# Kernel optimization log

Hardware: AMD Instinct MI355X
Metric: run time of the kernel (lower is better)

## Reference

```python
import jax, jax.numpy as jnp
import numpy as np

B, T, P, U = 2, 50, 5111, 64


def setup_inputs() -> dict:
    key = jax.random.key(0)
    ks = jax.random.split(key, 12)
    data_target = jax.random.randint(ks[0], (B, T), 0, P)
    data_cor = jax.random.randint(ks[1], (B, T), 0, 2)
    # X: bi-LSTM max-pooled problem encodings [P, 2U]
    X = jax.random.normal(ks[2], (P, 2 * U), dtype=jnp.float32) * 0.1
    # cos_X: cosine similarity of X with itself (as in call_encode)
    norm = jnp.sqrt(jnp.sum(X * X, axis=1))
    cos_X = (X @ X.T) / (norm[:, None] * norm[None, :])
    # causal lower-triangular aggregation mask [T, T]
    trimatrix = jnp.tril(jnp.ones((T, T), dtype=jnp.float32))
    # frozen embedding2 table [2, 4U]
    emb2 = jax.random.uniform(ks[3], (2, 4 * U), minval=-1.0, maxval=1.0, dtype=jnp.float32)
    # LSTM params (keras gate order i,f,c,o), input dim 4U
    s = 0.1549193338
    Wk = jax.random.uniform(ks[4], (4 * U, 4 * U), minval=-s, maxval=s, dtype=jnp.float32)
    Wr = jax.random.normal(ks[5], (U, 4 * U), dtype=jnp.float32) * 0.05  # orthogonal-ish stand-in
    bl = jnp.concatenate([jnp.zeros((U,)), jnp.ones((U,)), jnp.zeros((2 * U,))]).astype(jnp.float32)  # unit forget bias
    s1 = 0.1732050808
    W1 = jax.random.uniform(ks[6], (3 * U, 50), minval=-s1, maxval=s1, dtype=jnp.float32)
    b1 = jnp.zeros((50,), dtype=jnp.float32)
    s2 = 0.3429971703
    W2 = jax.random.uniform(ks[7], (50, 1), minval=-s2, maxval=s2, dtype=jnp.float32)
    b2 = jnp.zeros((1,), dtype=jnp.float32)
    return {"data_target": data_target, "data_cor": data_cor, "num_pro": P,
            "X": X, "cos_X": cos_X, "trimatrix": trimatrix, "emb2": emb2,
            "Wk": Wk, "Wr": Wr, "bl": bl, "W1": W1, "b1": b1, "W2": W2, "b2": b2}


def _lstm(x, Wk, Wr, bl):
    # x: [B, T, D] -> h: [B, T, U]; keras LSTM math, gate order i,f,g,o
    u = Wr.shape[0]
    xT = jnp.swapaxes(x, 0, 1)  # [T, B, D]
    h0 = jnp.zeros((x.shape[0], u), x.dtype)
    c0 = jnp.zeros((x.shape[0], u), x.dtype)

    def step(carry, xt):
        h, c = carry
        z = xt @ Wk + h @ Wr + bl
        i, f, g, o = jnp.split(z, 4, axis=-1)
        c = jax.nn.sigmoid(f) * c + jax.nn.sigmoid(i) * jnp.tanh(g)
        h = jax.nn.sigmoid(o) * jnp.tanh(c)
        return (h, c), h

    _, hs = jax.lax.scan(step, (h0, c0), xT)
    return jnp.swapaxes(hs, 0, 1)


def reference(data_target, data_cor, num_pro, X, cos_X, trimatrix, emb2, Wk, Wr, bl, W1, b1, W2, b2):
    # one_hot @ X == gather
    t_X = X[data_target]                             # [B,T,2U]
    t_X = jnp.concatenate([t_X, t_X], axis=-1)       # [B,T,4U]
    xt = t_X * emb2[data_cor]                        # [B,T,4U]
    ht = _lstm(xt, Wk, Wr, bl)                       # [B,T,U]
    # attention aggregation: a[b,t,p] = cos_X[target[b,t], p]
    a = cos_X[data_target]                           # [B,T,P]
    # ajhj[b,s,p,u] = sum_t trimatrix[t,s] * a[b,t,p] * ht[b,t,u]
    ajhj = jnp.einsum('btp,btu,ts->bspu', a, ht, trimatrix)  # [B,T,P,U]
    XX = jnp.broadcast_to(X[None, None], (ajhj.shape[0], ajhj.shape[1], num_pro, X.shape[1]))
    hatt = jnp.concatenate([ajhj, XX], axis=-1)      # [B,T,P,3U]
    r = jax.nn.relu(hatt @ W1 + b1)                  # [B,T,P,50]
    r = r @ W2 + b2                                  # [B,T,P,1]
    return r
```

## Files before the change

### kernel.cpp

```cpp
#include <hip/hip_runtime.h>
#include <math.h>

#define B_ 2
#define T_ 50
#define P_ 5111
#define U_ 64
#define SC_ 10
#define CH_ 5
#define NQ_ 1278
#define XWTB_ 254
#define OUT_BASE_ 256
#define OUTB_ 200
#define GRID_ (OUT_BASE_ + OUTB_)
#define MAGIC_ 0x5EED1E55

typedef float v2f __attribute__((ext_vector_type(2)));

#define QPERM(x, ctrl)                                                        \
  __int_as_float(__builtin_amdgcn_mov_dpp(__float_as_int(x), (ctrl), 0xf, 0xf, true))

__device__ __forceinline__ float ld_coh(const float* p) {
  return __hip_atomic_load(p, __ATOMIC_RELAXED, __HIP_MEMORY_SCOPE_AGENT);
}
__device__ __forceinline__ void st_coh(float* p, float v) {
  __hip_atomic_store(p, v, __ATOMIC_RELAXED, __HIP_MEMORY_SCOPE_AGENT);
}
__device__ __forceinline__ void wait_flag(const int* f) {
  while (__hip_atomic_load(f, __ATOMIC_RELAXED, __HIP_MEMORY_SCOPE_AGENT) != MAGIC_)
    __builtin_amdgcn_s_sleep(2);
}
__device__ __forceinline__ void set_flag(int* f) {
  __hip_atomic_store(f, MAGIC_, __ATOMIC_RELAXED, __HIP_MEMORY_SCOPE_AGENT);
}

union SMem {
  struct {
    float H[T_ + 1][64];
    union {
      float ZXs[T_][256];
      float W1s[64 * 50];
    } z;
  } lstm;
  float xe[256];
  float xrow[4][128];
  struct { float G[T_ * 50]; float W2s[50]; int tgt[T_]; } outr;
};

__device__ __forceinline__ void lstm_role(
    int b, SMem& sm, const float* ZX, const float* Wr, const float* bl,
    const float* W1, float* G, const int* zxflag, int* gflag) {
  const int k   = threadIdx.x;
  const int g   = k & 3;
  const int u   = k >> 2;
  const int col = g * 64 + u;

  v2f w2[32];
#pragma unroll
  for (int i = 0; i < 32; ++i) {
    v2f t; t.x = Wr[(2 * i) * 256 + col]; t.y = Wr[(2 * i + 1) * 256 + col];
    w2[i] = t;
  }
  const float blv = bl[col];
  if (k < 64) sm.lstm.H[0][k] = 0.f;
  if (k < T_) wait_flag(&zxflag[b * T_ + k]);
  __syncthreads();

  {
    float r[T_];
#pragma unroll
    for (int t = 0; t < T_; ++t) r[t] = ld_coh(&ZX[(b * T_ + t) * 256 + k]);
#pragma unroll
    for (int t = 0; t < T_; ++t) sm.lstm.z.ZXs[t][k] = r[t];
  }
  float w1r[13];
#pragma unroll
  for (int j = 0; j < 13; ++j) {
    const int i = k + j * 256;
    w1r[j] = (i < 64 * 50) ? W1[i] : 0.f;
  }
  __syncthreads();

  float c = 0.f;
  __builtin_amdgcn_s_setprio(1);
  for (int t = 0; t < T_; ++t) {
    const float zcur = sm.lstm.z.ZXs[t][col];
    const float4* h4 = (const float4*)&sm.lstm.H[t][0];
    v2f a0 = {0.f, 0.f}, a1 = {0.f, 0.f}, a2 = {0.f, 0.f}, a3 = {0.f, 0.f};
#pragma unroll
    for (int q = 0; q < 16; ++q) {
      const float4 hq = h4[q];
      v2f hlo; hlo.x = hq.x; hlo.y = hq.y;
      v2f hhi; hhi.x = hq.z; hhi.y = hq.w;
      if (q & 1) {
        a2 = __builtin_elementwise_fma(hlo, w2[2 * q], a2);
        a3 = __builtin_elementwise_fma(hhi, w2[2 * q + 1], a3);
      } else {
        a0 = __builtin_elementwise_fma(hlo, w2[2 * q], a0);
        a1 = __builtin_elementwise_fma(hhi, w2[2 * q + 1], a1);
      }
    }
    const v2f as = (a0 + a2) + (a1 + a3);
    const float z = as.x + as.y + zcur + blv;
    const bool isg2 = (g == 2);
    const float arg = isg2 ? (2.f * z) : (-z);
    const float e   = __expf(arg);
    const float v   = __fdividef(1.f, 1.f + e);
    const float res = isg2 ? fmaf(-2.f, v, 1.f) : v;
    const float v1 = QPERM(res, 177);
    const float v2 = QPERM(res, 78);
    const float v3 = QPERM(res, 27);
    const float ig = (g == 0) ? res : (g == 1) ? v1 : (g == 2) ? v2 : v3;
    const float fg = (g == 1) ? res : (g == 0) ? v1 : (g == 3) ? v2 : v3;
    const float gg = (g == 2) ? res : (g == 3) ? v1 : (g == 0) ? v2 : v3;
    const float og = (g == 3) ? res : (g == 2) ? v1 : (g == 1) ? v2 : v3;
    c = fmaf(fg, c, ig * gg);
    const float th = fmaf(-2.f, __fdividef(1.f, 1.f + __expf(2.f * c)), 1.f);
    if (g == 0) sm.lstm.H[t + 1][u] = og * th;
    __syncthreads();
  }
  __builtin_amdgcn_s_setprio(0);

#pragma unroll
  for (int j = 0; j < 13; ++j) {
    const int i = k + j * 256;
    if (i < 64 * 50) sm.lstm.z.W1s[i] = w1r[j];
  }
  __syncthreads();

  const v2f* W1_2 = (const v2f*)sm.lstm.z.W1s;
  for (int task = k; task < T_ * 25; task += 256) {
    const int t  = task / 25;
    const int jp = task % 25;
    const float* hrow = &sm.lstm.H[t + 1][0];
    v2f acc = {0.f, 0.f};
#pragma unroll
    for (int u2 = 0; u2 < 64; ++u2) {
      v2f hb; hb.x = hrow[u2]; hb.y = hrow[u2];
      acc = __builtin_elementwise_fma(hb, W1_2[u2 * 25 + jp], acc);
    }
    st_coh(&G[b * (T_ * 50) + 2 * task],     acc.x);
    st_coh(&G[b * (T_ * 50) + 2 * task + 1], acc.y);
  }
  __syncthreads();
  if (k == 0) set_flag(&gflag[b]);
}

__device__ __forceinline__ void prod_role(
    int blk, SMem& sm, const int* tgt, const int* cor, const float* X,
    const float* emb2, const float* Wk, const float* W1, const float* b1,
    float* ZX, float* XWT, int* zxflag, int* quadflag) {
  const int k = threadIdx.x;

  if (blk - 2 < B_ * T_) {
    const int bt = blk - 2;
    const int t_ = tgt[bt], c_ = cor[bt];
    sm.xe[k] = X[t_ * 128 + (k & 127)] * emb2[c_ * 256 + k];
    __syncthreads();
    float z = 0.f;
#pragma unroll 8
    for (int d = 0; d < 256; ++d)
      z = fmaf(sm.xe[d], Wk[d * 256 + k], z);
    st_coh(&ZX[bt * 256 + k], z);
    __syncthreads();
    if (k == 0) set_flag(&zxflag[bt]);
  }

  const int sub = k >> 6, lane = k & 63;
  const int stripe = (blk - 102 + XWTB_) % XWTB_;
  for (int q = stripe; q < NQ_; q += XWTB_) {
    const int p = q * 4 + sub;
    if (p < P_) {
      sm.xrow[sub][lane]      = X[p * 128 + lane];
      sm.xrow[sub][64 + lane] = X[p * 128 + 64 + lane];
    }
    __syncthreads();
    if (p < P_ && lane < 50) {
      float acc = b1[lane];
#pragma unroll 16
      for (int u = 0; u < 128; ++u)
        acc = fmaf(sm.xrow[sub][u], W1[(64 + u) * 50 + lane], acc);
      st_coh(&XWT[lane * P_ + p], acc);
    }
    __syncthreads();
    if (k == 0) set_flag(&quadflag[q]);
  }
}

template <int CH>
__device__ __forceinline__ void out_body(
    int pc, int b, SMem& sm, const int* tgt, const float* cosX,
    const float* G, const float* XWT, const float* W2, const float* b2,
    float* out, const int* gflag, const int* quadflag) {
  constexpr int s_lo = CH * SC_;
  constexpr int s_hi = s_lo + SC_;
  const int tid = threadIdx.x;
  const int p   = pc * 256 + tid;
  const bool act = (p < P_);

  if (tid < 50) {
    sm.outr.W2s[tid] = W2[tid];
    sm.outr.tgt[tid] = tgt[b * T_ + tid];
  }
  __syncthreads();

  float av[T_ - s_lo];
#pragma unroll
  for (int t = s_lo; t < T_; ++t)
    av[t - s_lo] = act ? cosX[sm.outr.tgt[t] * P_ + p] : 0.f;

  if (tid < 64) {
    const int q = pc * 64 + tid;
    if (q < NQ_) wait_flag(&quadflag[q]);
  }
  __syncthreads();

  v2f S2[25];
#pragma unroll
  for (int jj = 0; jj < 25; ++jj) {
    v2f t2;
    t2.x = act ? ld_coh(&XWT[(2 * jj) * P_ + p]) : 0.f;
    t2.y = act ? ld_coh(&XWT[(2 * jj + 1) * P_ + p]) : 0.f;
    S2[jj] = t2;
  }

  if (tid == 0) wait_flag(&gflag[b]);
  __syncthreads();
  for (int i = s_lo * 50 + tid; i < T_ * 50; i += 256)
    sm.outr.G[i] = ld_coh(&G[b * T_ * 50 + i]);
  __syncthreads();

#pragma unroll
  for (int t = T_ - 1; t >= s_hi; --t) {
    const v2f* G2 = (const v2f*)&sm.outr.G[t * 50];
    v2f av2; av2.x = av[t - s_lo]; av2.y = av[t - s_lo];
#pragma unroll
    for (int jj = 0; jj < 25; ++jj)
      S2[jj] = __builtin_elementwise_fma(av2, G2[jj], S2[jj]);
  }

  const v2f* W2_2 = (const v2f*)sm.outr.W2s;
  const float b2v = b2[0];
  const v2f zero2 = {0.f, 0.f};
#pragma unroll
  for (int s = s_hi - 1; s >= s_lo; --s) {
    const v2f* G2 = (const v2f*)&sm.outr.G[s * 50];
    v2f av2; av2.x = av[s - s_lo]; av2.y = av[s - s_lo];
    v2f acc2; acc2.x = b2v; acc2.y = 0.f;
#pragma unroll
    for (int jj = 0; jj < 25; ++jj) {
      S2[jj] = __builtin_elementwise_fma(av2, G2[jj], S2[jj]);
      const v2f r = __builtin_elementwise_max(S2[jj], zero2);
      acc2 = __builtin_elementwise_fma(r, W2_2[jj], acc2);
    }
    if (act) out[(b * T_ + s) * P_ + p] = acc2.x + acc2.y;
  }
}

__global__ __launch_bounds__(256) void mega_kernel(
    const int* __restrict__ tgt, const int* __restrict__ cor,
    const float* __restrict__ X, const float* __restrict__ cosX,
    const float* __restrict__ emb2, const float* __restrict__ Wk,
    const float* __restrict__ Wr, const float* __restrict__ bl,
    const float* __restrict__ W1, const float* __restrict__ b1,
    const float* __restrict__ W2, const float* __restrict__ b2,
    float* __restrict__ ZX, float* __restrict__ G, float* __restrict__ XWT,
    int* __restrict__ zxflag, int* __restrict__ gflag,
    int* __restrict__ quadflag, float* __restrict__ out) {
  __shared__ __align__(16) SMem sm;
  const int blk = blockIdx.x;

  if (blk < B_) {
    lstm_role(blk, sm, ZX, Wr, bl, W1, G, zxflag, gflag);
    return;
  }
  if (blk < OUT_BASE_) {
    prod_role(blk, sm, tgt, cor, X, emb2, Wk, W1, b1, ZX, XWT, zxflag, quadflag);
    return;
  }
  const int obi = blk - OUT_BASE_;
  const int pc  = obi % 20;
  const int b   = (obi / 20) & 1;
  switch (obi / 40) {
    case 0: out_body<0>(pc, b, sm, tgt, cosX, G, XWT, W2, b2, out, gflag, quadflag); break;
    case 1: out_body<1>(pc, b, sm, tgt, cosX, G, XWT, W2, b2, out, gflag, quadflag); break;
    case 2: out_body<2>(pc, b, sm, tgt, cosX, G, XWT, W2, b2, out, gflag, quadflag); break;
    case 3: out_body<3>(pc, b, sm, tgt, cosX, G, XWT, W2, b2, out, gflag, quadflag); break;
    default: out_body<4>(pc, b, sm, tgt, cosX, G, XWT, W2, b2, out, gflag, quadflag); break;
  }
}

extern "C" void kernel_launch(void* const* d_in, const int* in_sizes, int n_in,
                              void* d_out, int out_size, void* d_ws, size_t ws_size,
                              hipStream_t stream) {
  const int*   tgt  = (const int*)d_in[0];
  const int*   cor  = (const int*)d_in[1];
  const float* X    = (const float*)d_in[3];
  const float* cosX = (const float*)d_in[4];
  const float* emb2 = (const float*)d_in[6];
  const float* Wk   = (const float*)d_in[7];
  const float* Wr   = (const float*)d_in[8];
  const float* bl   = (const float*)d_in[9];
  const float* W1   = (const float*)d_in[10];
  const float* b1   = (const float*)d_in[11];
  const float* W2   = (const float*)d_in[12];
  const float* b2   = (const float*)d_in[13];
  float* out = (float*)d_out;

  float* ws  = (float*)d_ws;
  float* ZX  = ws;
  float* G   = ws + 25600;
  float* XWT = ws + 30600;
  int*   fl  = (int*)(ws + 286150);
  int* zxflag   = fl;
  int* gflag    = fl + 100;
  int* quadflag = fl + 102;

  mega_kernel<<<dim3(GRID_), dim3(256), 0, stream>>>(
      tgt, cor, X, cosX, emb2, Wk, Wr, bl, W1, b1, W2, b2,
      ZX, G, XWT, zxflag, gflag, quadflag, out);
}
```

Baseline: 217.0 us.

## Compute LSTM recurrence on two waves with two gate columns per thread

Restructures the serial LSTM recurrence so 128 threads (two waves) each compute two gate columns instead of 256 threads computing one. The gate exchange shrinks to a single DPP permute per pair. The other two waves load W1 into registers, stay in step with the per-timestep barriers, then stage W1 to shared memory. This is meant to cut the latency of each recurrent step, which sits on the critical path, though each thread now does twice the FMAs and holds twice the weight registers. A launch-bounds hint of two blocks per SM is also added, which can limit register allocation.

```diff
diff --git a/kernel.cpp b/kernel.cpp
--- a/kernel.cpp
+++ b/kernel.cpp
@@ -49,18 +49,8 @@
 __device__ __forceinline__ void lstm_role(
     int b, SMem& sm, const float* ZX, const float* Wr, const float* bl,
     const float* W1, float* G, const int* zxflag, int* gflag) {
-  const int k   = threadIdx.x;
-  const int g   = k & 3;
-  const int u   = k >> 2;
-  const int col = g * 64 + u;
-
-  v2f w2[32];
-#pragma unroll
-  for (int i = 0; i < 32; ++i) {
-    v2f t; t.x = Wr[(2 * i) * 256 + col]; t.y = Wr[(2 * i + 1) * 256 + col];
-    w2[i] = t;
-  }
-  const float blv = bl[col];
+  const int k = threadIdx.x;
+
   if (k < 64) sm.lstm.H[0][k] = 0.f;
   if (k < T_) wait_flag(&zxflag[b * T_ + k]);
   __syncthreads();
@@ -72,60 +62,86 @@
 #pragma unroll
     for (int t = 0; t < T_; ++t) sm.lstm.z.ZXs[t][k] = r[t];
   }
-  float w1r[13];
-#pragma unroll
-  for (int j = 0; j < 13; ++j) {
-    const int i = k + j * 256;
-    w1r[j] = (i < 64 * 50) ? W1[i] : 0.f;
-  }
-  __syncthreads();
-
-  float c = 0.f;
-  __builtin_amdgcn_s_setprio(1);
-  for (int t = 0; t < T_; ++t) {
-    const float zcur = sm.lstm.z.ZXs[t][col];
-    const float4* h4 = (const float4*)&sm.lstm.H[t][0];
-    v2f a0 = {0.f, 0.f}, a1 = {0.f, 0.f}, a2 = {0.f, 0.f}, a3 = {0.f, 0.f};
-#pragma unroll
-    for (int q = 0; q < 16; ++q) {
-      const float4 hq = h4[q];
-      v2f hlo; hlo.x = hq.x; hlo.y = hq.y;
-      v2f hhi; hhi.x = hq.z; hhi.y = hq.w;
-      if (q & 1) {
-        a2 = __builtin_elementwise_fma(hlo, w2[2 * q], a2);
-        a3 = __builtin_elementwise_fma(hhi, w2[2 * q + 1], a3);
-      } else {
-        a0 = __builtin_elementwise_fma(hlo, w2[2 * q], a0);
-        a1 = __builtin_elementwise_fma(hhi, w2[2 * q + 1], a1);
+
+  if (k < 128) {
+    const int u    = k >> 1;
+    const int pair = k & 1;
+    const int colA = pair * 128 + u;
+    const int colB = pair * 128 + 64 + u;
+
+    v2f wA[32], wB[32];
+#pragma unroll
+    for (int i = 0; i < 32; ++i) {
+      v2f ta; ta.x = Wr[(2 * i) * 256 + colA]; ta.y = Wr[(2 * i + 1) * 256 + colA];
+      wA[i] = ta;
+      v2f tb; tb.x = Wr[(2 * i) * 256 + colB]; tb.y = Wr[(2 * i + 1) * 256 + colB];
+      wB[i] = tb;
+    }
+    const float blvA = bl[colA];
+    const float blvB = bl[colB];
+    __syncthreads();
+
+    float c = 0.f;
+    __builtin_amdgcn_s_setprio(1);
+    for (int t = 0; t < T_; ++t) {
+      const float zAcur = sm.lstm.z.ZXs[t][colA];
+      const float zBcur = sm.lstm.z.ZXs[t][colB];
+      const float4* h4 = (const float4*)&sm.lstm.H[t][0];
+      v2f a0 = {0.f, 0.f}, a1 = {0.f, 0.f}, a2 = {0.f, 0.f}, a3 = {0.f, 0.f};
+      v2f b0 = {0.f, 0.f}, b1 = {0.f, 0.f}, b2 = {0.f, 0.f}, b3 = {0.f, 0.f};
+#pragma unroll
+      for (int q = 0; q < 16; ++q) {
+        const float4 hq = h4[q];
+        v2f hlo; hlo.x = hq.x; hlo.y = hq.y;
+        v2f hhi; hhi.x = hq.z; hhi.y = hq.w;
+        if (q & 1) {
+          a2 = __builtin_elementwise_fma(hlo, wA[2 * q], a2);
+          a3 = __builtin_elementwise_fma(hhi, wA[2 * q + 1], a3);
+          b2 = __builtin_elementwise_fma(hlo, wB[2 * q], b2);
+          b3 = __builtin_elementwise_fma(hhi, wB[2 * q + 1], b3);
+        } else {
+          a0 = __builtin_elementwise_fma(hlo, wA[2 * q], a0);
+          a1 = __builtin_elementwise_fma(hhi, wA[2 * q + 1], a1);
+          b0 = __builtin_elementwise_fma(hlo, wB[2 * q], b0);
+          b1 = __builtin_elementwise_fma(hhi, wB[2 * q + 1], b1);
+        }
       }
-    }
-    const v2f as = (a0 + a2) + (a1 + a3);
-    const float z = as.x + as.y + zcur + blv;
-    const bool isg2 = (g == 2);
-    const float arg = isg2 ? (2.f * z) : (-z);
-    const float e   = __expf(arg);
-    const float v   = __fdividef(1.f, 1.f + e);
-    const float res = isg2 ? fmaf(-2.f, v, 1.f) : v;
-    const float v1 = QPERM(res, 177);
-    const float v2 = QPERM(res, 78);
-    const float v3 = QPERM(res, 27);
-    const float ig = (g == 0) ? res : (g == 1) ? v1 : (g == 2) ? v2 : v3;
-    const float fg = (g == 1) ? res : (g == 0) ? v1 : (g == 3) ? v2 : v3;
-    const float gg = (g == 2) ? res : (g == 3) ? v1 : (g == 0) ? v2 : v3;
-    const float og = (g == 3) ? res : (g == 2) ? v1 : (g == 1) ? v2 : v3;
-    c = fmaf(fg, c, ig * gg);
-    const float th = fmaf(-2.f, __fdividef(1.f, 1.f + __expf(2.f * c)), 1.f);
-    if (g == 0) sm.lstm.H[t + 1][u] = og * th;
-    __syncthreads();
-  }
-  __builtin_amdgcn_s_setprio(0);
-
-#pragma unroll
-  for (int j = 0; j < 13; ++j) {
-    const int i = k + j * 256;
-    if (i < 64 * 50) sm.lstm.z.W1s[i] = w1r[j];
-  }
-  __syncthreads();
+      const v2f asA = (a0 + a2) + (a1 + a3);
+      const v2f asB = (b0 + b2) + (b1 + b3);
+      const float zA = asA.x + asA.y + zAcur + blvA;
+      const float zB = asB.x + asB.y + zBcur + blvB;
+
+      const bool isg2 = (pair == 1);
+      const float argA = isg2 ? (2.f * zA) : (-zA);
+      const float eA   = __expf(argA);
+      const float vA   = __fdividef(1.f, 1.f + eA);
+      const float resA = isg2 ? fmaf(-2.f, vA, 1.f) : vA;
+      const float eB   = __expf(-zB);
+      const float resB = __fdividef(1.f, 1.f + eB);
+
+      const float xA = QPERM(resA, 177);
+      const float xB = QPERM(resB, 177);
+      const float ig = isg2 ? xA : resA;
+      const float fg = isg2 ? xB : resB;
+      const float gg = isg2 ? resA : xA;
+
+      c = fmaf(fg, c, ig * gg);
+      const float th = fmaf(-2.f, __fdividef(1.f, 1.f + __expf(2.f * c)), 1.f);
+      if (isg2) sm.lstm.H[t + 1][u] = resB * th;
+      __syncthreads();
+    }
+    __builtin_amdgcn_s_setprio(0);
+    __syncthreads();
+  } else {
+    float w1r[25];
+#pragma unroll
+    for (int j = 0; j < 25; ++j) w1r[j] = W1[(k - 128) + j * 128];
+    __syncthreads();
+    for (int t = 0; t < T_; ++t) __syncthreads();
+#pragma unroll
+    for (int j = 0; j < 25; ++j) sm.lstm.z.W1s[(k - 128) + j * 128] = w1r[j];
+    __syncthreads();
+  }
 
   const v2f* W1_2 = (const v2f*)sm.lstm.z.W1s;
   for (int task = k; task < T_ * 25; task += 256) {
@@ -256,7 +272,7 @@
   }
 }
 
-__global__ __launch_bounds__(256) void mega_kernel(
+__global__ __launch_bounds__(256, 2) void mega_kernel(
     const int* __restrict__ tgt, const int* __restrict__ cor,
     const float* __restrict__ X, const float* __restrict__ cosX,
     const float* __restrict__ emb2, const float* __restrict__ Wk,
```

New measurement: 225.2 us. +3.8%, slower.

## Split producer work into a separate kernel launch instead of flag-synchronized roles

Applied to the files above, without the earlier changes.

Moves the ZX projection and X·W1 precompute out of the persistent mega-kernel into a standalone producer kernel with one block per row or quad. The consumer kernel then runs the LSTM and output blocks without waiting on zxflag or quadflag, relying on stream ordering instead. This removes spin-waits and coherent atomic loads and stores, and gives the XWT precompute many more blocks. The cost is an extra kernel launch and losing overlap between producer and consumer work. The gflag handshake between LSTM and output blocks remains.

```diff
diff --git a/kernel.cpp b/kernel.cpp
--- a/kernel.cpp
+++ b/kernel.cpp
@@ -8,10 +8,6 @@
 #define SC_ 10
 #define CH_ 5
 #define NQ_ 1278
-#define XWTB_ 254
-#define OUT_BASE_ 256
-#define OUTB_ 200
-#define GRID_ (OUT_BASE_ + OUTB_)
 #define MAGIC_ 0x5EED1E55
 
 typedef float v2f __attribute__((ext_vector_type(2)));
@@ -33,7 +29,47 @@
   __hip_atomic_store(f, MAGIC_, __ATOMIC_RELAXED, __HIP_MEMORY_SCOPE_AGENT);
 }
 
-union SMem {
+__global__ __launch_bounds__(256) void prod_kernel(
+    const int* __restrict__ tgt, const int* __restrict__ cor,
+    const float* __restrict__ X, const float* __restrict__ emb2,
+    const float* __restrict__ Wk, const float* __restrict__ W1,
+    const float* __restrict__ b1, float* __restrict__ ZX,
+    float* __restrict__ XWT) {
+  const int blk = blockIdx.x;
+  const int k   = threadIdx.x;
+  __shared__ float smem[516];
+
+  if (blk < B_ * T_) {
+    const int t_ = tgt[blk], c_ = cor[blk];
+    smem[k] = X[t_ * 128 + (k & 127)] * emb2[c_ * 256 + k];
+    __syncthreads();
+    float z = 0.f;
+#pragma unroll 8
+    for (int d = 0; d < 256; ++d)
+      z = fmaf(smem[d], Wk[d * 256 + k], z);
+    ZX[blk * 256 + k] = z;
+    return;
+  }
+
+  const int q    = blk - B_ * T_;
+  const int sub  = k >> 6, lane = k & 63;
+  const int p    = q * 4 + sub;
+  float* xrow = &smem[sub * 129];
+  if (p < P_) {
+    xrow[lane]      = X[p * 128 + lane];
+    xrow[64 + lane] = X[p * 128 + 64 + lane];
+  }
+  __syncthreads();
+  if (p < P_ && lane < 50) {
+    float acc = b1[lane];
+#pragma unroll 16
+    for (int u = 0; u < 128; ++u)
+      acc = fmaf(xrow[u], W1[(64 + u) * 50 + lane], acc);
+    XWT[lane * P_ + p] = acc;
+  }
+}
+
+union SMemC {
   struct {
     float H[T_ + 1][64];
     union {
@@ -41,14 +77,12 @@
       float W1s[64 * 50];
     } z;
   } lstm;
-  float xe[256];
-  float xrow[4][128];
   struct { float G[T_ * 50]; float W2s[50]; int tgt[T_]; } outr;
 };
 
 __device__ __forceinline__ void lstm_role(
-    int b, SMem& sm, const float* ZX, const float* Wr, const float* bl,
-    const float* W1, float* G, const int* zxflag, int* gflag) {
+    int b, SMemC& sm, const float* ZX, const float* Wr, const float* bl,
+    const float* W1, float* G, int* gflag) {
   const int k   = threadIdx.x;
   const int g   = k & 3;
   const int u   = k >> 2;
@@ -62,13 +96,11 @@
   }
   const float blv = bl[col];
   if (k < 64) sm.lstm.H[0][k] = 0.f;
-  if (k < T_) wait_flag(&zxflag[b * T_ + k]);
-  __syncthreads();
 
   {
     float r[T_];
 #pragma unroll
-    for (int t = 0; t < T_; ++t) r[t] = ld_coh(&ZX[(b * T_ + t) * 256 + k]);
+    for (int t = 0; t < T_; ++t) r[t] = ZX[(b * T_ + t) * 256 + k];
 #pragma unroll
     for (int t = 0; t < T_; ++t) sm.lstm.z.ZXs[t][k] = r[t];
   }
@@ -145,52 +177,11 @@
   if (k == 0) set_flag(&gflag[b]);
 }
 
-__device__ __forceinline__ void prod_role(
-    int blk, SMem& sm, const int* tgt, const int* cor, const float* X,
-    const float* emb2, const float* Wk, const float* W1, const float* b1,
-    float* ZX, float* XWT, int* zxflag, int* quadflag) {
-  const int k = threadIdx.x;
-
-  if (blk - 2 < B_ * T_) {
-    const int bt = blk - 2;
-    const int t_ = tgt[bt], c_ = cor[bt];
-    sm.xe[k] = X[t_ * 128 + (k & 127)] * emb2[c_ * 256 + k];
-    __syncthreads();
-    float z = 0.f;
-#pragma unroll 8
-    for (int d = 0; d < 256; ++d)
-      z = fmaf(sm.xe[d], Wk[d * 256 + k], z);
-    st_coh(&ZX[bt * 256 + k], z);
-    __syncthreads();
-    if (k == 0) set_flag(&zxflag[bt]);
-  }
-
-  const int sub = k >> 6, lane = k & 63;
-  const int stripe = (blk - 102 + XWTB_) % XWTB_;
-  for (int q = stripe; q < NQ_; q += XWTB_) {
-    const int p = q * 4 + sub;
-    if (p < P_) {
-      sm.xrow[sub][lane]      = X[p * 128 + lane];
-      sm.xrow[sub][64 + lane] = X[p * 128 + 64 + lane];
-    }
-    __syncthreads();
-    if (p < P_ && lane < 50) {
-      float acc = b1[lane];
-#pragma unroll 16
-      for (int u = 0; u < 128; ++u)
-        acc = fmaf(sm.xrow[sub][u], W1[(64 + u) * 50 + lane], acc);
-      st_coh(&XWT[lane * P_ + p], acc);
-    }
-    __syncthreads();
-    if (k == 0) set_flag(&quadflag[q]);
-  }
-}
-
 template <int CH>
 __device__ __forceinline__ void out_body(
-    int pc, int b, SMem& sm, const int* tgt, const float* cosX,
+    int pc, int b, SMemC& sm, const int* tgt, const float* cosX,
     const float* G, const float* XWT, const float* W2, const float* b2,
-    float* out, const int* gflag, const int* quadflag) {
+    float* out, const int* gflag) {
   constexpr int s_lo = CH * SC_;
   constexpr int s_hi = s_lo + SC_;
   const int tid = threadIdx.x;
@@ -208,18 +199,12 @@
   for (int t = s_lo; t < T_; ++t)
     av[t - s_lo] = act ? cosX[sm.outr.tgt[t] * P_ + p] : 0.f;
 
-  if (tid < 64) {
-    const int q = pc * 64 + tid;
-    if (q < NQ_) wait_flag(&quadflag[q]);
-  }
-  __syncthreads();
-
   v2f S2[25];
 #pragma unroll
   for (int jj = 0; jj < 25; ++jj) {
     v2f t2;
-    t2.x = act ? ld_coh(&XWT[(2 * jj) * P_ + p]) : 0.f;
-    t2.y = act ? ld_coh(&XWT[(2 * jj + 1) * P_ + p]) : 0.f;
+    t2.x = act ? XWT[(2 * jj) * P_ + p] : 0.f;
+    t2.y = act ? XWT[(2 * jj + 1) * P_ + p] : 0.f;
     S2[jj] = t2;
   }
 
@@ -256,36 +241,29 @@
   }
 }
 
-__global__ __launch_bounds__(256) void mega_kernel(
-    const int* __restrict__ tgt, const int* __restrict__ cor,
-    const float* __restrict__ X, const float* __restrict__ cosX,
-    const float* __restrict__ emb2, const float* __restrict__ Wk,
+__global__ __launch_bounds__(256) void cons_kernel(
+    const int* __restrict__ tgt, const float* __restrict__ cosX,
     const float* __restrict__ Wr, const float* __restrict__ bl,
-    const float* __restrict__ W1, const float* __restrict__ b1,
-    const float* __restrict__ W2, const float* __restrict__ b2,
-    float* __restrict__ ZX, float* __restrict__ G, float* __restrict__ XWT,
-    int* __restrict__ zxflag, int* __restrict__ gflag,
-    int* __restrict__ quadflag, float* __restrict__ out) {
-  __shared__ __align__(16) SMem sm;
+    const float* __restrict__ W1, const float* __restrict__ W2,
+    const float* __restrict__ b2, const float* __restrict__ ZX,
+    float* __restrict__ G, const float* __restrict__ XWT,
+    int* __restrict__ gflag, float* __restrict__ out) {
+  __shared__ __align__(16) SMemC sm;
   const int blk = blockIdx.x;
 
   if (blk < B_) {
-    lstm_role(blk, sm, ZX, Wr, bl, W1, G, zxflag, gflag);
+    lstm_role(blk, sm, ZX, Wr, bl, W1, G, gflag);
     return;
   }
-  if (blk < OUT_BASE_) {
-    prod_role(blk, sm, tgt, cor, X, emb2, Wk, W1, b1, ZX, XWT, zxflag, quadflag);
-    return;
-  }
-  const int obi = blk - OUT_BASE_;
+  const int obi = blk - B_;
   const int pc  = obi % 20;
   const int b   = (obi / 20) & 1;
   switch (obi / 40) {
-    case 0: out_body<0>(pc, b, sm, tgt, cosX, G, XWT, W2, b2, out, gflag, quadflag); break;
-    case 1: out_body<1>(pc, b, sm, tgt, cosX, G, XWT, W2, b2, out, gflag, quadflag); break;
-    case 2: out_body<2>(pc, b, sm, tgt, cosX, G, XWT, W2, b2, out, gflag, quadflag); break;
-    case 3: out_body<3>(pc, b, sm, tgt, cosX, G, XWT, W2, b2, out, gflag, quadflag); break;
-    default: out_body<4>(pc, b, sm, tgt, cosX, G, XWT, W2, b2, out, gflag, quadflag); break;
+    case 0: out_body<0>(pc, b, sm, tgt, cosX, G, XWT, W2, b2, out, gflag); break;
+    case 1: out_body<1>(pc, b, sm, tgt, cosX, G, XWT, W2, b2, out, gflag); break;
+    case 2: out_body<2>(pc, b, sm, tgt, cosX, G, XWT, W2, b2, out, gflag); break;
+    case 3: out_body<3>(pc, b, sm, tgt, cosX, G, XWT, W2, b2, out, gflag); break;
+    default: out_body<4>(pc, b, sm, tgt, cosX, G, XWT, W2, b2, out, gflag); break;
   }
 }
 
@@ -310,12 +288,10 @@
   float* ZX  = ws;
   float* G   = ws + 25600;
   float* XWT = ws + 30600;
-  int*   fl  = (int*)(ws + 286150);
-  int* zxflag   = fl;
-  int* gflag    = fl + 100;
-  int* quadflag = fl + 102;
-
-  mega_kernel<<<dim3(GRID_), dim3(256), 0, stream>>>(
-      tgt, cor, X, cosX, emb2, Wk, Wr, bl, W1, b1, W2, b2,
-      ZX, G, XWT, zxflag, gflag, quadflag, out);
-}
+  int*   gflag = (int*)(ws + 286150);
+
+  prod_kernel<<<dim3(B_ * T_ + NQ_), dim3(256), 0, stream>>>(
+      tgt, cor, X, emb2, Wk, W1, b1, ZX, XWT);
+  cons_kernel<<<dim3(B_ + 200), dim3(256), 0, stream>>>(
+      tgt, cosX, Wr, bl, W1, W2, b2, ZX, G, XWT, gflag, out);
+}
```

Measured after the change: 256.3 us. 18.1% more time.
